# Optimization experiments

Hardware: AMD Instinct MI355X
Metric: run time of the kernel (lower is better)

The kernel has to match this reference:

```python
import jax, jax.numpy as jnp
import numpy as np

CTX_WIN = 5
PAD = (CTX_WIN - 1) // 2


def setup_inputs() -> dict:
    key = jax.random.key(0)
    k1, k2, k3 = jax.random.split(key, 3)
    B, S, H, A = 64, 1024, 128, 8
    return {
        "batch_docIn": jax.random.normal(k1, (B, S, H), dtype=jnp.float32),
        "aspEmbed_weight": jax.random.uniform(k2, (A, CTX_WIN * H), dtype=jnp.float32, minval=-0.01, maxval=0.01),
        "aspProj": jax.random.uniform(k3, (A, H, H), dtype=jnp.float32, minval=-0.01, maxval=0.01),
    }


def reference(batch_docIn, aspEmbed_weight, aspProj):
    B, S, H = batch_docIn.shape
    A = aspProj.shape[0]
    # Per-aspect projection: (A, B, S, H)
    proj = jnp.einsum('bsh,ahf->absf', batch_docIn, aspProj)
    E = aspEmbed_weight.reshape(A, H, CTX_WIN)
    # Zero-pad along seq, then accumulate windowed scores without materializing
    padded = jnp.pad(proj, ((0, 0), (0, 0), (PAD, PAD), (0, 0)))
    attn = sum(
        jnp.einsum('absh,ah->abs',
                   jax.lax.dynamic_slice_in_dim(padded, w, S, axis=2),
                   E[:, :, w])
        for w in range(CTX_WIN)
    )  # (A, B, S)
    attn = jax.nn.softmax(attn, axis=2)  # softmax over seq (torch dim=1)
    rep = jnp.einsum('absh,abs->abh', proj, attn)  # (A, B, H)
    # outputs: attn (B, A, S), rep (B, A, H)
    return attn.transpose(1, 0, 2), rep.transpose(1, 0, 2)
```

## Files before the change

kernel.cpp:

```cpp
#include <hip/hip_runtime.h>
#include <hip/hip_bf16.h>

#define S_DIM 1024
#define H_DIM 128
#define A_DIM 8
#define W_WIN 5

typedef unsigned int uint;
typedef unsigned short ushort;
typedef __attribute__((ext_vector_type(8))) short short8;
typedef __attribute__((ext_vector_type(4))) float f32x4;

union U128 { uint4 u; short8 s; };

__device__ __forceinline__ ushort f2bf(float f) {
    uint u = __float_as_uint(f);
    uint r = (u + 0x7fffu + ((u >> 16) & 1u)) >> 16;
    return (ushort)r;
}

__global__ __launch_bounds__(128) void k_g(const float* __restrict__ P,
                                           const float* __restrict__ We,
                                           ushort* __restrict__ Gt) {
    const int a  = blockIdx.y;
    const int hc = blockIdx.x;
    const int t  = threadIdx.x;

    __shared__ float Es[H_DIM * W_WIN];
    __shared__ float red[16 * 8 * W_WIN];
    for (int i = t; i < H_DIM * W_WIN; i += 128) Es[i] = We[a * (H_DIM * W_WIN) + i];
    __syncthreads();

    const int hl = t >> 3, fo = t & 7;
    const float* Pr = P + ((size_t)(a * H_DIM + hc * 16 + hl)) * H_DIM + fo * 16;
    float acc[W_WIN] = {0.f, 0.f, 0.f, 0.f, 0.f};
#pragma unroll
    for (int j4 = 0; j4 < 4; ++j4) {
        float4 pv = ((const float4*)Pr)[j4];
        float pj[4] = {pv.x, pv.y, pv.z, pv.w};
#pragma unroll
        for (int j = 0; j < 4; ++j) {
            const float* e = &Es[(fo * 16 + j4 * 4 + j) * W_WIN];
#pragma unroll
            for (int w = 0; w < W_WIN; ++w) acc[w] += pj[j] * e[w];
        }
    }
#pragma unroll
    for (int w = 0; w < W_WIN; ++w) red[(hl * 8 + fo) * W_WIN + w] = acc[w];
    __syncthreads();

    if (t < 80) {
        const int w = t >> 4, h2 = t & 15;
        float s = 0.f;
#pragma unroll
        for (int f8 = 0; f8 < 8; ++f8) s += red[(h2 * 8 + f8) * W_WIN + w];
        Gt[a * (W_WIN * H_DIM) + w * H_DIM + hc * 16 + h2] = f2bf(s);
    }
}

#define CS 64
#define RROWS (CS + 4)
#define EPITCH 88
__global__ __launch_bounds__(256) void k_scores(const float* __restrict__ Din,
                                                const ushort* __restrict__ Gt,
                                                ushort* __restrict__ escore,
                                                float* __restrict__ numPart,
                                                float* __restrict__ Zpart) {
    __shared__ uint4 Dl[RROWS * 16];
    __shared__ uint4 Gl[9 * 80];
    __shared__ ushort el[16 * EPITCH];
    __shared__ float Zw[32];
    const int b   = blockIdx.y;
    const int slc = blockIdx.x;
    const int s0  = slc * CS;
    const int t   = threadIdx.x;
    const float* Db = Din + (size_t)b * S_DIM * H_DIM;

    {
        const int c  = t & 15;
        const int r0 = t >> 4;
        float4 va[5], vb[5];
        bool ok[5];
#pragma unroll
        for (int k = 0; k < 4; ++k) {
            const int gs = s0 - 2 + r0 + k * 16;
            ok[k] = (gs >= 0) && (gs < S_DIM);
            const int gc = min(max(gs, 0), S_DIM - 1);
            const float4* p = (const float4*)(Db + (size_t)gc * H_DIM + c * 8);
            va[k] = p[0];
            vb[k] = p[1];
        }
        if (t < 64) {
            const int gs = s0 - 2 + 64 + r0;
            ok[4] = (gs >= 0) && (gs < S_DIM);
            const int gc = min(max(gs, 0), S_DIM - 1);
            const float4* p = (const float4*)(Db + (size_t)gc * H_DIM + c * 8);
            va[4] = p[0];
            vb[4] = p[1];
        }
#pragma unroll
        for (int k = 0; k < 5; ++k) {
            if (k == 4 && t >= 64) break;
            const int r = (k == 4) ? (64 + r0) : (r0 + k * 16);
            float4 A = va[k], Bv = vb[k];
            if (!ok[k]) { A = make_float4(0.f,0.f,0.f,0.f); Bv = A; }
            uint4 q;
            q.x = (uint)f2bf(A.x)  | ((uint)f2bf(A.y)  << 16);
            q.y = (uint)f2bf(A.z)  | ((uint)f2bf(A.w)  << 16);
            q.z = (uint)f2bf(Bv.x) | ((uint)f2bf(Bv.y) << 16);
            q.w = (uint)f2bf(Bv.z) | ((uint)f2bf(Bv.w) << 16);
            Dl[r * 16 + (c ^ (r & 15))] = q;
        }
    }
    {
        const uint4* Gg = (const uint4*)Gt;
        for (int i = t; i < 9 * 80; i += 256) {
            const int n = i / 80, c = i - n * 80;
            uint4 v = make_uint4(0u, 0u, 0u, 0u);
            if (n < 8) v = Gg[n * 80 + c];
            Gl[n * 80 + ((c & ~15) | ((c & 15) ^ n))] = v;
        }
    }
    __syncthreads();

    const int lane = t & 63;
    const int wv   = t >> 6;
    const int lm   = lane & 15;
    const int lq   = lane >> 4;
    const int gr   = (lm < 8) ? lm : 8;

    f32x4 acc0 = {0.f, 0.f, 0.f, 0.f};
#pragma unroll
    for (int kk = 0; kk < 20; ++kk) {
        const int w = kk >> 2;
        const int r0 = wv * 16 + lm + w;
        const int cidx = (kk & 3) * 4 + lq;
        const int gc = kk * 4 + lq;
        U128 av, bv;
        bv.u = Gl[gr * 80 + ((gc & ~15) | ((gc & 15) ^ gr))];
        av.u = Dl[r0 * 16 + (cidx ^ (r0 & 15))];
        acc0 = __builtin_amdgcn_mfma_f32_16x16x32_bf16(av.s, bv.s, acc0, 0, 0, 0);
    }

    float4 e0;
    e0.x = __expf(acc0.x); e0.y = __expf(acc0.y); e0.z = __expf(acc0.z); e0.w = __expf(acc0.w);
    uint2 d0;
    d0.x = (uint)f2bf(e0.x) | ((uint)f2bf(e0.y) << 16);
    d0.y = (uint)f2bf(e0.z) | ((uint)f2bf(e0.w) << 16);
    const int sb = wv * 16 + lq * 4;
    if (lm < A_DIM)
        *(uint2*)(escore + (((size_t)b * A_DIM + lm) << 10) + s0 + sb) = d0;
    *(uint2*)(&el[lm * EPITCH + sb]) = d0;

    float es = e0.x + e0.y + e0.z + e0.w;
    es += __shfl_xor(es, 16);
    es += __shfl_xor(es, 32);
    if (lq == 0 && lm < A_DIM) Zw[wv * 8 + lm] = es;
    __syncthreads();

    const ushort* Dls = (const ushort*)Dl;
    U128 afr[2];
#pragma unroll
    for (int kk = 0; kk < 2; ++kk)
        afr[kk].u = *(const uint4*)(&el[lm * EPITCH + kk * 32 + lq * 8]);

    f32x4 accN[2] = {{0.f,0.f,0.f,0.f},{0.f,0.f,0.f,0.f}};
#pragma unroll
    for (int nt = 0; nt < 2; ++nt) {
        const int h  = wv * 32 + nt * 16 + lm;
        const int ch = h >> 3, hw = h & 7;
#pragma unroll
        for (int kk = 0; kk < 2; ++kk) {
            uint p[4];
#pragma unroll
            for (int jj = 0; jj < 4; ++jj) {
                const int sj = kk * 32 + lq * 8 + jj * 2;
                const int ra = sj + 2, rb = sj + 3;
                const uint lo = Dls[(ra * 16 + (ch ^ (ra & 15))) * 8 + hw];
                const uint hi = Dls[(rb * 16 + (ch ^ (rb & 15))) * 8 + hw];
                p[jj] = lo | (hi << 16);
            }
            U128 bfr; bfr.u = make_uint4(p[0], p[1], p[2], p[3]);
            accN[nt] = __builtin_amdgcn_mfma_f32_16x16x32_bf16(afr[kk].s, bfr.s, accN[nt], 0, 0, 0);
        }
    }

    if (lq < 2) {
#pragma unroll
        for (int nt = 0; nt < 2; ++nt) {
            const int h = wv * 32 + nt * 16 + lm;
#pragma unroll
            for (int r = 0; r < 4; ++r)
                numPart[(((size_t)(b * 16 + slc) * 8) + lq * 4 + r) * H_DIM + h] = accN[nt][r];
        }
    }
    if (t < A_DIM)
        Zpart[(b * 16 + slc) * 8 + t] = Zw[t] + Zw[8 + t] + Zw[16 + t] + Zw[24 + t];
}

__global__ __launch_bounds__(128) void k_final(const ushort* __restrict__ escore,
                                               const float* __restrict__ numPart,
                                               const float* __restrict__ Zpart,
                                               const float* __restrict__ P,
                                               float* __restrict__ attn,
                                               float* __restrict__ rep) {
    __shared__ float ws[H_DIM];
    __shared__ float par[128];
    const int ba = blockIdx.y;
    const int hf = blockIdx.x;
    const int b = ba >> 3, a = ba & 7;
    const int t = threadIdx.x;

    float Zs = 0.f;
#pragma unroll
    for (int k = 0; k < 16; ++k) Zs += Zpart[(b * 16 + k) * 8 + a];
    const float rz = 1.0f / Zs;

    float s = 0.f;
#pragma unroll
    for (int k = 0; k < 16; ++k)
        s += numPart[(((size_t)(b * 16 + k) * 8) + a) * H_DIM + t];
    ws[t] = s * rz;

    const ushort* ep = escore + (size_t)ba * S_DIM;
    float* ap = attn + (size_t)ba * S_DIM;
    {
        uint2 q = *(const uint2*)(ep + hf * 512 + t * 4);
        float4 v;
        v.x = __uint_as_float(q.x << 16) * rz;
        v.y = __uint_as_float(q.x & 0xffff0000u) * rz;
        v.z = __uint_as_float(q.y << 16) * rz;
        v.w = __uint_as_float(q.y & 0xffff0000u) * rz;
        *(float4*)(ap + hf * 512 + t * 4) = v;
    }
    __syncthreads();

    const int f  = hf * 64 + (t & 63);
    const int h0 = (t >> 6) * 64;
    const float* Pa = P + (size_t)a * H_DIM * H_DIM + f;
    float acc = 0.f;
#pragma unroll 16
    for (int hh = 0; hh < 64; ++hh)
        acc += ws[h0 + hh] * Pa[(size_t)(h0 + hh) * H_DIM];
    par[t] = acc;
    __syncthreads();
    if (t < 64)
        rep[(size_t)ba * H_DIM + f] = par[t] + par[t + 64];
}

extern "C" void kernel_launch(void* const* d_in, const int* in_sizes, int n_in,
                              void* d_out, int out_size, void* d_ws, size_t ws_size,
                              hipStream_t stream) {
    const float* docIn = (const float*)d_in[0];
    const float* We    = (const float*)d_in[1];
    const float* P     = (const float*)d_in[2];
    float* out = (float*)d_out;

    const int B = in_sizes[0] / (S_DIM * H_DIM);

    ushort* Gt     = (ushort*)d_ws;
    ushort* escore = (ushort*)((char*)d_ws + 32768);
    float* numPart = (float*)((char*)d_ws + 32768 +
                              (size_t)B * A_DIM * S_DIM * 2);
    float* Zpart   = numPart + (size_t)B * 16 * 8 * H_DIM;

    k_g<<<dim3(8, 8), 128, 0, stream>>>(P, We, Gt);
    k_scores<<<dim3(S_DIM / CS, B), 256, 0, stream>>>(docIn, Gt, escore, numPart, Zpart);
    k_final<<<dim3(2, B * A_DIM), 128, 0, stream>>>(escore, numPart, Zpart, P, out,
                                                    out + (size_t)B * A_DIM * S_DIM);
}
```

Before: 89.10 us.

## Double score-kernel sequence chunk to 128 and merge final kernel halves

Raises the k_scores sequence chunk from 64 to 128 rows with 512 threads per block. This halves the number of blocks, the partial numerator/Z outputs and the halo reloads. k_final now has one block per (batch, aspect) that covers the full H output and both attention halves, so the cross-thread partial-sum reduction goes away. The cost is fewer blocks in flight (512 score blocks) and a longer serial 128-step dot product per thread in the final kernel.

After: 87.57 us. Within noise of the previous version (-1.7%).

```diff
diff --git a/kernel.cpp b/kernel.cpp
--- a/kernel.cpp
+++ b/kernel.cpp
@@ -58,10 +58,10 @@
     }
 }
 
-#define CS 64
+#define CS 128
 #define RROWS (CS + 4)
-#define EPITCH 88
-__global__ __launch_bounds__(256) void k_scores(const float* __restrict__ Din,
+#define EPITCH 136
+__global__ __launch_bounds__(512) void k_scores(const float* __restrict__ Din,
                                                 const ushort* __restrict__ Gt,
                                                 ushort* __restrict__ escore,
                                                 float* __restrict__ numPart,
@@ -69,7 +69,7 @@
     __shared__ uint4 Dl[RROWS * 16];
     __shared__ uint4 Gl[9 * 80];
     __shared__ ushort el[16 * EPITCH];
-    __shared__ float Zw[32];
+    __shared__ float Zw[64];
     const int b   = blockIdx.y;
     const int slc = blockIdx.x;
     const int s0  = slc * CS;
@@ -83,7 +83,7 @@
         bool ok[5];
 #pragma unroll
         for (int k = 0; k < 4; ++k) {
-            const int gs = s0 - 2 + r0 + k * 16;
+            const int gs = s0 - 2 + r0 + k * 32;
             ok[k] = (gs >= 0) && (gs < S_DIM);
             const int gc = min(max(gs, 0), S_DIM - 1);
             const float4* p = (const float4*)(Db + (size_t)gc * H_DIM + c * 8);
@@ -91,7 +91,7 @@
             vb[k] = p[1];
         }
         if (t < 64) {
-            const int gs = s0 - 2 + 64 + r0;
+            const int gs = s0 - 2 + 128 + r0;
             ok[4] = (gs >= 0) && (gs < S_DIM);
             const int gc = min(max(gs, 0), S_DIM - 1);
             const float4* p = (const float4*)(Db + (size_t)gc * H_DIM + c * 8);
@@ -101,7 +101,7 @@
 #pragma unroll
         for (int k = 0; k < 5; ++k) {
             if (k == 4 && t >= 64) break;
-            const int r = (k == 4) ? (64 + r0) : (r0 + k * 16);
+            const int r = (k == 4) ? (128 + r0) : (r0 + k * 32);
             float4 A = va[k], Bv = vb[k];
             if (!ok[k]) { A = make_float4(0.f,0.f,0.f,0.f); Bv = A; }
             uint4 q;
@@ -114,7 +114,7 @@
     }
     {
         const uint4* Gg = (const uint4*)Gt;
-        for (int i = t; i < 9 * 80; i += 256) {
+        for (int i = t; i < 9 * 80; i += 512) {
             const int n = i / 80, c = i - n * 80;
             uint4 v = make_uint4(0u, 0u, 0u, 0u);
             if (n < 8) v = Gg[n * 80 + c];
@@ -159,18 +159,17 @@
     __syncthreads();
 
     const ushort* Dls = (const ushort*)Dl;
-    U128 afr[2];
-#pragma unroll
-    for (int kk = 0; kk < 2; ++kk)
+    U128 afr[4];
+#pragma unroll
+    for (int kk = 0; kk < 4; ++kk)
         afr[kk].u = *(const uint4*)(&el[lm * EPITCH + kk * 32 + lq * 8]);
 
-    f32x4 accN[2] = {{0.f,0.f,0.f,0.f},{0.f,0.f,0.f,0.f}};
-#pragma unroll
-    for (int nt = 0; nt < 2; ++nt) {
-        const int h  = wv * 32 + nt * 16 + lm;
+    f32x4 accN = {0.f, 0.f, 0.f, 0.f};
+    {
+        const int h  = wv * 16 + lm;
         const int ch = h >> 3, hw = h & 7;
 #pragma unroll
-        for (int kk = 0; kk < 2; ++kk) {
+        for (int kk = 0; kk < 4; ++kk) {
             uint p[4];
 #pragma unroll
             for (int jj = 0; jj < 4; ++jj) {
@@ -181,21 +180,22 @@
                 p[jj] = lo | (hi << 16);
             }
             U128 bfr; bfr.u = make_uint4(p[0], p[1], p[2], p[3]);
-            accN[nt] = __builtin_amdgcn_mfma_f32_16x16x32_bf16(afr[kk].s, bfr.s, accN[nt], 0, 0, 0);
+            accN = __builtin_amdgcn_mfma_f32_16x16x32_bf16(afr[kk].s, bfr.s, accN, 0, 0, 0);
         }
     }
 
     if (lq < 2) {
-#pragma unroll
-        for (int nt = 0; nt < 2; ++nt) {
-            const int h = wv * 32 + nt * 16 + lm;
-#pragma unroll
-            for (int r = 0; r < 4; ++r)
-                numPart[(((size_t)(b * 16 + slc) * 8) + lq * 4 + r) * H_DIM + h] = accN[nt][r];
-        }
-    }
-    if (t < A_DIM)
-        Zpart[(b * 16 + slc) * 8 + t] = Zw[t] + Zw[8 + t] + Zw[16 + t] + Zw[24 + t];
+        const int h = wv * 16 + lm;
+#pragma unroll
+        for (int r = 0; r < 4; ++r)
+            numPart[(((size_t)(b * 8 + slc) * 8) + lq * 4 + r) * H_DIM + h] = accN[r];
+    }
+    if (t < A_DIM) {
+        float z = 0.f;
+#pragma unroll
+        for (int k = 0; k < 8; ++k) z += Zw[k * 8 + t];
+        Zpart[(b * 8 + slc) * 8 + t] = z;
+    }
 }
 
 __global__ __launch_bounds__(128) void k_final(const ushort* __restrict__ escore,
@@ -205,47 +205,41 @@
                                                float* __restrict__ attn,
                                                float* __restrict__ rep) {
     __shared__ float ws[H_DIM];
-    __shared__ float par[128];
-    const int ba = blockIdx.y;
-    const int hf = blockIdx.x;
+    const int ba = blockIdx.x;
     const int b = ba >> 3, a = ba & 7;
     const int t = threadIdx.x;
 
     float Zs = 0.f;
 #pragma unroll
-    for (int k = 0; k < 16; ++k) Zs += Zpart[(b * 16 + k) * 8 + a];
+    for (int k = 0; k < 8; ++k) Zs += Zpart[(b * 8 + k) * 8 + a];
     const float rz = 1.0f / Zs;
 
     float s = 0.f;
 #pragma unroll
-    for (int k = 0; k < 16; ++k)
-        s += numPart[(((size_t)(b * 16 + k) * 8) + a) * H_DIM + t];
+    for (int k = 0; k < 8; ++k)
+        s += numPart[(((size_t)(b * 8 + k) * 8) + a) * H_DIM + t];
     ws[t] = s * rz;
 
     const ushort* ep = escore + (size_t)ba * S_DIM;
     float* ap = attn + (size_t)ba * S_DIM;
-    {
-        uint2 q = *(const uint2*)(ep + hf * 512 + t * 4);
+#pragma unroll
+    for (int i = 0; i < 2; ++i) {
+        uint2 q = *(const uint2*)(ep + i * 512 + t * 4);
         float4 v;
         v.x = __uint_as_float(q.x << 16) * rz;
         v.y = __uint_as_float(q.x & 0xffff0000u) * rz;
         v.z = __uint_as_float(q.y << 16) * rz;
         v.w = __uint_as_float(q.y & 0xffff0000u) * rz;
-        *(float4*)(ap + hf * 512 + t * 4) = v;
-    }
-    __syncthreads();
-
-    const int f  = hf * 64 + (t & 63);
-    const int h0 = (t >> 6) * 64;
-    const float* Pa = P + (size_t)a * H_DIM * H_DIM + f;
+        *(float4*)(ap + i * 512 + t * 4) = v;
+    }
+    __syncthreads();
+
+    const float* Pa = P + (size_t)a * H_DIM * H_DIM + t;
     float acc = 0.f;
-#pragma unroll 16
-    for (int hh = 0; hh < 64; ++hh)
-        acc += ws[h0 + hh] * Pa[(size_t)(h0 + hh) * H_DIM];
-    par[t] = acc;
-    __syncthreads();
-    if (t < 64)
-        rep[(size_t)ba * H_DIM + f] = par[t] + par[t + 64];
+#pragma unroll 32
+    for (int hh = 0; hh < H_DIM; ++hh)
+        acc += ws[hh] * Pa[(size_t)hh * H_DIM];
+    rep[(size_t)ba * H_DIM + t] = acc;
 }
 
 extern "C" void kernel_launch(void* const* d_in, const int* in_sizes, int n_in,
@@ -262,10 +256,10 @@
     ushort* escore = (ushort*)((char*)d_ws + 32768);
     float* numPart = (float*)((char*)d_ws + 32768 +
                               (size_t)B * A_DIM * S_DIM * 2);
-    float* Zpart   = numPart + (size_t)B * 16 * 8 * H_DIM;
+    float* Zpart   = numPart + (size_t)B * 8 * 8 * H_DIM;
 
     k_g<<<dim3(8, 8), 128, 0, stream>>>(P, We, Gt);
-    k_scores<<<dim3(S_DIM / CS, B), 256, 0, stream>>>(docIn, Gt, escore, numPart, Zpart);
-    k_final<<<dim3(2, B * A_DIM), 128, 0, stream>>>(escore, numPart, Zpart, P, out,
-                                                    out + (size_t)B * A_DIM * S_DIM);
-}
+    k_scores<<<dim3(S_DIM / CS, B), 512, 0, stream>>>(docIn, Gt, escore, numPart, Zpart);
+    k_final<<<B * A_DIM, 128, 0, stream>>>(escore, numPart, Zpart, P, out,
+                                           out + (size_t)B * A_DIM * S_DIM);
+}
```
